# Kernel optimization log

Hardware: AMD Instinct MI355X
Metric: run time of the kernel (lower is better)

The kernel has to match this reference:

```python
import jax, jax.numpy as jnp
import numpy as np

BANDWIDTH = 0.5  # init kwarg


def setup_inputs() -> dict:
    key = jax.random.key(0)
    k1, k2 = jax.random.split(key)
    samples = jax.random.normal(k1, (2, 4096, 6), dtype=jnp.float32)    # [B, N, D]
    locations = jax.random.normal(k2, (2048, 6), dtype=jnp.float32)    # [L, D]
    return {"samples": samples, "locations": locations}


def reference(samples, locations):
    # Pairwise squared distances: ||samples - locations||^2 over D
    # torch: norm(...)**2 == sum of squares (same math, cleaner gradient)
    d = samples[None, :, :, :] - locations[:, None, None, :]   # [L, B, N, D]
    diff2 = jnp.sum(d * d, axis=-1)                            # [L, B, N]
    out = jnp.exp(-diff2 / (2.0 * BANDWIDTH ** 2)).sum(axis=-1)  # [L, B]
    norm = out.sum(axis=0)                                     # [B]
    # torch broadcasting of [L,B] / [1,1,B] yields [1,L,B]
    pdf = out / norm.reshape(1, 1, -1)                          # [1, L, B]
    return pdf
```

## Files before the change

### kernel.cpp

```cpp
#include <hip/hip_runtime.h>


#define KDE_B 2
#define KDE_N 4096
#define KDE_D 6
#define KDE_L 2048

#define NEG2_LOG2E (-2.8853900817779268f)

#define TL 128
#define LPT 4
#define NC 256
#define NCHUNK (KDE_N / NC)
#define LTILES (KDE_L / TL)

__global__ void __launch_bounds__(256, 2)
kde_main_kernel(const float* __restrict__ samples,
                const float* __restrict__ locations,
                float* __restrict__ wsum,
                float* __restrict__ wnorm) {
    const int bid = blockIdx.x;
    const int b  = bid & 1;
    const int c  = (bid >> 1) & (NCHUNK - 1);
    const int lt = bid >> 5;

    const int tid = threadIdx.x;
    const int g   = tid >> 3;
    const int sub = tid & 7;

    __shared__ float lds[NC * 8];

    {
        const float* sp = samples + ((size_t)b * KDE_N + (size_t)c * NC + tid) * KDE_D;
        float2 s01 = *reinterpret_cast<const float2*>(sp);
        float2 s23 = *reinterpret_cast<const float2*>(sp + 2);
        float2 s45 = *reinterpret_cast<const float2*>(sp + 4);
        float s2 = s01.x * s01.x;
        s2 = fmaf(s01.y, s01.y, s2);
        s2 = fmaf(s23.x, s23.x, s2);
        s2 = fmaf(s23.y, s23.y, s2);
        s2 = fmaf(s45.x, s45.x, s2);
        s2 = fmaf(s45.y, s45.y, s2);
        float4* dst = reinterpret_cast<float4*>(&lds[tid * 8]);
        dst[0] = make_float4(s01.x, s01.y, s23.x, s23.y);
        dst[1] = make_float4(s45.x, s45.y, NEG2_LOG2E * s2, 0.f);
    }

    const int lbase = lt * TL + g * LPT;
    float lp[LPT][KDE_D];
    float A[LPT];
#pragma unroll
    for (int j = 0; j < LPT; ++j) {
        const float* q = locations + (size_t)(lbase + j) * KDE_D;
        float2 q01 = *reinterpret_cast<const float2*>(q);
        float2 q23 = *reinterpret_cast<const float2*>(q + 2);
        float2 q45 = *reinterpret_cast<const float2*>(q + 4);
        float l2 = q01.x * q01.x;
        l2 = fmaf(q01.y, q01.y, l2);
        l2 = fmaf(q23.x, q23.x, l2);
        l2 = fmaf(q23.y, q23.y, l2);
        l2 = fmaf(q45.x, q45.x, l2);
        l2 = fmaf(q45.y, q45.y, l2);
        const float m = -2.0f * NEG2_LOG2E;
        lp[j][0] = m * q01.x; lp[j][1] = m * q01.y;
        lp[j][2] = m * q23.x; lp[j][3] = m * q23.y;
        lp[j][4] = m * q45.x; lp[j][5] = m * q45.y;
        A[j] = NEG2_LOG2E * l2;
    }

    float acc[LPT] = {0.f, 0.f, 0.f, 0.f};

    __syncthreads();

    const float4* lds4 = reinterpret_cast<const float4*>(lds);
#pragma unroll 4
    for (int k = 0; k < NC / 8; ++k) {
        const int n = (k << 3) | sub;
        float4 sA = lds4[n * 2];
        float4 sB = lds4[n * 2 + 1];
#pragma unroll
        for (int j = 0; j < LPT; ++j) {
            float e = fmaf(sA.x, lp[j][0], A[j]);
            e = fmaf(sA.y, lp[j][1], e);
            e = fmaf(sA.z, lp[j][2], e);
            e = fmaf(sA.w, lp[j][3], e);
            e = fmaf(sB.x, lp[j][4], e);
            e = fmaf(sB.y, lp[j][5], e);
            e += sB.z;
            acc[j] += __builtin_amdgcn_exp2f(e);
        }
    }

#pragma unroll
    for (int j = 0; j < LPT; ++j) {
        float v = acc[j];
        v += __shfl_xor(v, 1, 64);
        v += __shfl_xor(v, 2, 64);
        v += __shfl_xor(v, 4, 64);
        acc[j] = v;
    }

    float tot = 0.f;
    if (sub == 0) {
#pragma unroll
        for (int j = 0; j < LPT; ++j) {
            atomicAdd(&wsum[(size_t)(lbase + j) * KDE_B + b], acc[j]);
            tot += acc[j];
        }
    }

    tot += __shfl_xor(tot, 8, 64);
    tot += __shfl_xor(tot, 16, 64);
    tot += __shfl_xor(tot, 32, 64);
    __shared__ float wred[4];
    if ((tid & 63) == 0) wred[tid >> 6] = tot;
    __syncthreads();
    if (tid == 0) atomicAdd(&wnorm[b], wred[0] + wred[1] + wred[2] + wred[3]);
}

__global__ void kde_scale_kernel(const float* __restrict__ wsum,
                                 const float* __restrict__ wnorm,
                                 float* __restrict__ out) {
    const int i = blockIdx.x * 256 + threadIdx.x;
    out[i] = wsum[i] / wnorm[i & 1];
}

extern "C" void kernel_launch(void* const* d_in, const int* in_sizes, int n_in,
                              void* d_out, int out_size, void* d_ws, size_t ws_size,
                              hipStream_t stream) {
    const float* samples   = (const float*)d_in[0];
    const float* locations = (const float*)d_in[1];
    float* out   = (float*)d_out;
    float* wsum  = (float*)d_ws;
    float* wnorm = (float*)d_ws + KDE_L * KDE_B;

    const int blocks = LTILES * NCHUNK * KDE_B;
    kde_main_kernel<<<blocks, 256, 0, stream>>>(samples, locations, wsum, wnorm);
    kde_scale_kernel<<<KDE_L * KDE_B / 256, 256, 0, stream>>>(wsum, wnorm, out);
}
```

Before: 66.33 us.

## Replace per-location atomics with partial-sum buffer reduced in scale kernel

```diff
diff --git a/kernel.cpp b/kernel.cpp
--- a/kernel.cpp
+++ b/kernel.cpp
@@ -13,11 +13,12 @@
 #define NC 256
 #define NCHUNK (KDE_N / NC)
 #define LTILES (KDE_L / TL)
+#define NBLOCKS (LTILES * NCHUNK * KDE_B)
 
 __global__ void __launch_bounds__(256, 2)
 kde_main_kernel(const float* __restrict__ samples,
                 const float* __restrict__ locations,
-                float* __restrict__ wsum,
+                float* __restrict__ wpart,
                 float* __restrict__ wnorm) {
     const int bid = blockIdx.x;
     const int b  = bid & 1;
@@ -28,7 +29,8 @@
     const int g   = tid >> 3;
     const int sub = tid & 7;
 
-    __shared__ float lds[NC * 8];
+    __shared__ float4 ldsA[NC];
+    __shared__ float4 ldsB[NC];
 
     {
         const float* sp = samples + ((size_t)b * KDE_N + (size_t)c * NC + tid) * KDE_D;
@@ -41,9 +43,8 @@
         s2 = fmaf(s23.y, s23.y, s2);
         s2 = fmaf(s45.x, s45.x, s2);
         s2 = fmaf(s45.y, s45.y, s2);
-        float4* dst = reinterpret_cast<float4*>(&lds[tid * 8]);
-        dst[0] = make_float4(s01.x, s01.y, s23.x, s23.y);
-        dst[1] = make_float4(s45.x, s45.y, NEG2_LOG2E * s2, 0.f);
+        ldsA[tid] = make_float4(s01.x, s01.y, s23.x, s23.y);
+        ldsB[tid] = make_float4(s45.x, s45.y, NEG2_LOG2E * s2, 0.f);
     }
 
     const int lbase = lt * TL + g * LPT;
@@ -72,12 +73,11 @@
 
     __syncthreads();
 
-    const float4* lds4 = reinterpret_cast<const float4*>(lds);
 #pragma unroll 4
     for (int k = 0; k < NC / 8; ++k) {
         const int n = (k << 3) | sub;
-        float4 sA = lds4[n * 2];
-        float4 sB = lds4[n * 2 + 1];
+        float4 sA = ldsA[n];
+        float4 sB = ldsB[n];
 #pragma unroll
         for (int j = 0; j < LPT; ++j) {
             float e = fmaf(sA.x, lp[j][0], A[j]);
@@ -104,7 +104,7 @@
     if (sub == 0) {
 #pragma unroll
         for (int j = 0; j < LPT; ++j) {
-            atomicAdd(&wsum[(size_t)(lbase + j) * KDE_B + b], acc[j]);
+            wpart[((size_t)b * NCHUNK + c) * KDE_L + lbase + j] = acc[j];
             tot += acc[j];
         }
     }
@@ -118,11 +118,18 @@
     if (tid == 0) atomicAdd(&wnorm[b], wred[0] + wred[1] + wred[2] + wred[3]);
 }
 
-__global__ void kde_scale_kernel(const float* __restrict__ wsum,
+__global__ void kde_scale_kernel(const float* __restrict__ wpart,
                                  const float* __restrict__ wnorm,
                                  float* __restrict__ out) {
-    const int i = blockIdx.x * 256 + threadIdx.x;
-    out[i] = wsum[i] / wnorm[i & 1];
+    const int gid = blockIdx.x * 256 + threadIdx.x;
+    const int l = gid >> 1;
+    const int b = gid & 1;
+    const float* base = wpart + (size_t)b * NCHUNK * KDE_L + l;
+    float s = 0.f;
+#pragma unroll
+    for (int c = 0; c < NCHUNK; ++c)
+        s += base[c * KDE_L];
+    out[gid] = s / wnorm[b];
 }
 
 extern "C" void kernel_launch(void* const* d_in, const int* in_sizes, int n_in,
@@ -131,10 +138,10 @@
     const float* samples   = (const float*)d_in[0];
     const float* locations = (const float*)d_in[1];
     float* out   = (float*)d_out;
-    float* wsum  = (float*)d_ws;
-    float* wnorm = (float*)d_ws + KDE_L * KDE_B;
+    float* ws    = (float*)d_ws;
+    float* wpart = ws;
+    float* wnorm = ws + KDE_B * NCHUNK * KDE_L;
 
-    const int blocks = LTILES * NCHUNK * KDE_B;
-    kde_main_kernel<<<blocks, 256, 0, stream>>>(samples, locations, wsum, wnorm);
-    kde_scale_kernel<<<KDE_L * KDE_B / 256, 256, 0, stream>>>(wsum, wnorm, out);
+    kde_main_kernel<<<NBLOCKS, 256, 0, stream>>>(samples, locations, wpart, wnorm);
+    kde_scale_kernel<<<KDE_L * KDE_B / 256, 256, 0, stream>>>(wpart, wnorm, out);
 }
```

Result: no change. 66.90 us (+0.9%).
